# Optimization experiments

Hardware: AMD Instinct MI355X
Metric: run time of the kernel (lower is better)

Reference implementation:

```python
import jax, jax.numpy as jnp
import numpy as np

EPS = 1e-5
K_NUM, EDGE_TYPE = 5, 2  # k_num = A_fixed_partitions(3) + edge_type(2)


def _bn(x, gamma, beta):
    # training-mode BatchNorm2d: batch stats over (N, T, V) per channel
    m = jnp.mean(x, axis=(0, 2, 3), keepdims=True)
    v = jnp.var(x, axis=(0, 2, 3), keepdims=True)
    return (x - m) * jax.lax.rsqrt(v + EPS) * gamma[None, :, None, None] + beta[None, :, None, None]


def setup_inputs() -> dict:
    key = jax.random.key(0)
    ks = jax.random.split(key, 6)
    N, C, T, V = 32, 64, 300, 25
    Cout, Kt = 64, 9
    x = jax.random.normal(ks[0], (N, C, T, V), jnp.float32)
    A = jax.random.uniform(ks[1], (K_NUM - EDGE_TYPE, V, V), jnp.float32) / V  # fixed adjacency (already scaled by edge_importance)
    B = jax.random.uniform(ks[2], (N, EDGE_TYPE, V, V), jnp.float32) / V      # per-sample adaptive adjacency A_act
    lamda_act = jnp.full((1,), 0.5, jnp.float32)
    conv_w = jax.random.normal(ks[3], (Cout * K_NUM, C), jnp.float32) * (1.0 / np.sqrt(C))  # 1x1 conv weight
    conv_b = jnp.zeros((Cout * K_NUM,), jnp.float32)
    bn1_g = jnp.ones((Cout,), jnp.float32)
    bn1_b = jnp.zeros((Cout,), jnp.float32)
    tcn_w = jax.random.normal(ks[4], (Cout, Cout, Kt, 1), jnp.float32) * (1.0 / np.sqrt(Cout * Kt))
    tcn_b = jnp.zeros((Cout,), jnp.float32)
    bn2_g = jnp.ones((Cout,), jnp.float32)
    bn2_b = jnp.zeros((Cout,), jnp.float32)
    return dict(x=x, A=A, B=B, lamda_act=lamda_act, conv_w=conv_w, conv_b=conv_b,
                bn1_g=bn1_g, bn1_b=bn1_b, tcn_w=tcn_w, tcn_b=tcn_b, bn2_g=bn2_g, bn2_b=bn2_b)


def reference(x, A, B, lamda_act, conv_w, conv_b, bn1_g, bn1_b, tcn_w, tcn_b, bn2_g, bn2_b):
    n, c, t, v = x.shape
    res = x  # identity residual (in_ch == out_ch, stride 1)
    # SpatialGcn: 1x1 conv (pure channel GEMM) -> split -> dual einsum graph conv
    y = jnp.einsum('nctv,oc->notv', x, conv_w) + conv_b[None, :, None, None]  # (n, K*Cout, t, v)
    cout = y.shape[1] // K_NUM
    y = y.reshape(n, K_NUM, cout, t, v)
    x1 = jnp.einsum('nkctv,kvw->nctw', y[:, :K_NUM - EDGE_TYPE], A)   # fixed adjacency
    x2 = jnp.einsum('nkctv,nkvw->nctw', y[:, K_NUM - EDGE_TYPE:], B)  # adaptive adjacency
    g = x1 + x2 * lamda_act[0]
    # tcn: BN -> ReLU -> temporal conv (9,1) pad (4,0) -> BN -> Dropout(0)=identity
    h = jax.nn.relu(_bn(g, bn1_g, bn1_b))
    h = jax.lax.conv_general_dilated(h, tcn_w, window_strides=(1, 1),
                                     padding=((4, 4), (0, 0)),
                                     dimension_numbers=('NCHW', 'OIHW', 'NCHW'))
    h = h + tcn_b[None, :, None, None]
    h = _bn(h, bn2_g, bn2_b)
    return jax.nn.relu(h + res)
```

## Files before the change

### kernel.cpp

```cpp
#include <hip/hip_runtime.h>
#include <hip/hip_bf16.h>

#define N_  32
#define C_  64
#define T_  300
#define V_  25
#define TV  (T_*V_)
#define CTV (C_*TV)
#define NELEM (N_*CTV)
#define CNTF 240000.0f

typedef float f32x4 __attribute__((ext_vector_type(4)));
typedef short bf16x8 __attribute__((ext_vector_type(8)));
typedef short s4v __attribute__((ext_vector_type(4)));
typedef short s8v __attribute__((ext_vector_type(8)));

__device__ __forceinline__ unsigned short f2bf(float f) {
    unsigned u = __float_as_uint(f);
    unsigned r = u + 0x7fffu + ((u >> 16) & 1u);
    return (unsigned short)(r >> 16);
}
__device__ __forceinline__ float bf2f(unsigned short u) {
    return __uint_as_float(((unsigned)u) << 16);
}
__device__ __forceinline__ unsigned cvt_pk(float lo, float hi) {
    unsigned r;
    asm("v_cvt_pk_bf16_f32 %0, %1, %2" : "=v"(r) : "v"(lo), "v"(hi));
    return r;
}

__global__ __launch_bounds__(256) void k_prep(
    const float* __restrict__ conv_w, const float* __restrict__ tw,
    unsigned short* __restrict__ w2b, unsigned short* __restrict__ twb)
{
    int tid = blockIdx.x*256 + threadIdx.x;
    for (int e = tid; e < 20480; e += 8192) {
        int ks = e >> 11, c = (e >> 5) & 63, kk = e & 31;
        w2b[e] = f2bf(conv_w[(((ks>>1)*64 + c)*64) + (ks&1)*32 + kk]);
    }
    for (int e = tid; e < 36864; e += 8192) {
        int gi = e >> 11, c = (e >> 5) & 63, kk = e & 31;
        int dt = gi >> 1, ks = gi & 1;
        twb[e] = f2bf(tw[(c*64 + 32*ks + kk)*9 + dt]);
    }
}

__global__ __launch_bounds__(256) void k_gcn(
    const float* __restrict__ x, const float* __restrict__ A,
    const float* __restrict__ B, const float* __restrict__ lamda,
    const unsigned short* __restrict__ w2b, const float* __restrict__ conv_b,
    unsigned short* __restrict__ gout, float* __restrict__ stats3)
{
    __shared__ unsigned short ash[5*32*40];
    __shared__ unsigned short zsh[32*328];
    __shared__ float csum[160];
    __shared__ float sbc[320];

    const int tb = blockIdx.x, n = blockIdx.y;
    const int t0 = tb*10;
    const int tid = threadIdx.x;
    const int lane = tid & 63, wv = tid >> 6;
    const int lg = lane >> 4, lr = lane & 15;
    const int crow = lr + 16*wv;
    const int cbase = 16*wv + 4*lg;

    bf16x8 wfrag[10];
    #pragma unroll
    for (int ks = 0; ks < 10; ++ks)
        wfrag[ks] = *(const bf16x8*)&w2b[(ks*64 + crow)*32 + 8*lg];

    const float lam = lamda[0];
    {
        s8v z8 = {0,0,0,0,0,0,0,0};
        for (int e = tid; e < 800; e += 256) *(s8v*)&ash[e*8] = z8;
    }
    for (int e = tid; e < 320; e += 256) sbc[e] = conv_b[e];
    __syncthreads();
    for (int e = tid; e < 3125; e += 256) {
        int k = e / 625, r = e - k*625;
        int v = r / 25, w = r - v*25;
        float val = (k < 3) ? A[e] : lam * B[((n<<1) + (k-3))*625 + r];
        ash[k*1280 + w*40 + v] = f2bf(val);
    }
    __syncthreads();
    for (int e = tid; e < 160; e += 256) {
        int k = e / 32, w = e % 32;
        float s = 0.f;
        for (int v = 0; v < 25; ++v) s += bf2f(ash[k*1280 + w*40 + v]);
        csum[e] = s;
    }
    __syncthreads();

    float bs0[4], bs1[4];
    #pragma unroll
    for (int r = 0; r < 4; ++r) {
        float s0 = 0.f, s1 = 0.f;
        #pragma unroll
        for (int k = 0; k < 5; ++k) {
            float cb = sbc[k*64 + cbase + r];
            s0 += cb * csum[k*32 + lr];
            s1 += cb * csum[k*32 + lr + 16];
        }
        bs0[r] = s0; bs1[r] = s1;
    }

    float sacc[4] = {0,0,0,0}, qacc[4] = {0,0,0,0};

    const float* xrow = x + n*CTV + crow*TV + t0*V_;
    float xf[8];
    #pragma unroll
    for (int i = 0; i < 8; ++i) { int v = 8*lg + i; xf[i] = (v < 25) ? xrow[v] : 0.f; }

    for (int tl = 0; tl < 10; ++tl) {
        union { bf16x8 v; unsigned u[4]; } xu;
        #pragma unroll
        for (int p = 0; p < 4; ++p) xu.u[p] = cvt_pk(xf[2*p], xf[2*p+1]);
        bf16x8 xfrag = xu.v;
        if (tl < 9) {
            const float* xn = xrow + (tl+1)*V_;
            #pragma unroll
            for (int i = 0; i < 8; ++i) { int v = 8*lg + i; xf[i] = (v < 25) ? xn[v] : 0.f; }
        }
        #pragma unroll
        for (int k = 0; k < 5; ++k)
        #pragma unroll
        for (int nt = 0; nt < 2; ++nt) {
            bf16x8 bfrag = *(const bf16x8*)&ash[k*1280 + (lr + 16*nt)*40 + 8*lg];
            f32x4 z = {0.f,0.f,0.f,0.f};
            z = __builtin_amdgcn_mfma_f32_16x16x32_bf16(xfrag, bfrag, z, 0, 0, 0);
            uint2 zz;
            zz.x = cvt_pk(z[0], z[1]);
            zz.y = cvt_pk(z[2], z[3]);
            *(uint2*)&zsh[(lr + 16*nt)*328 + k*64 + 16*wv + 4*lg] = zz;
        }
        __syncthreads();
        f32x4 acc0 = {0.f,0.f,0.f,0.f}, acc1 = {0.f,0.f,0.f,0.f};
        #pragma unroll
        for (int ks = 0; ks < 10; ++ks) {
            bf16x8 b0 = *(const bf16x8*)&zsh[lr*328 + 32*ks + 8*lg];
            bf16x8 b1 = *(const bf16x8*)&zsh[(lr+16)*328 + 32*ks + 8*lg];
            acc0 = __builtin_amdgcn_mfma_f32_16x16x32_bf16(wfrag[ks], b0, acc0, 0, 0, 0);
            acc1 = __builtin_amdgcn_mfma_f32_16x16x32_bf16(wfrag[ks], b1, acc1, 0, 0, 0);
        }
        float v0a[4], v1a[4];
        #pragma unroll
        for (int r = 0; r < 4; ++r) {
            v0a[r] = acc0[r] + bs0[r];
            v1a[r] = acc1[r] + bs1[r];
            sacc[r] += v0a[r] + (lr < 9 ? v1a[r] : 0.f);
            qacc[r] += v0a[r]*v0a[r] + (lr < 9 ? v1a[r]*v1a[r] : 0.f);
        }
        unsigned short* grow = gout + (size_t)(n*300 + t0 + tl)*1600;
        uint2 g0, g1;
        g0.x = cvt_pk(v0a[0], v0a[1]); g0.y = cvt_pk(v0a[2], v0a[3]);
        g1.x = cvt_pk(v1a[0], v1a[1]); g1.y = cvt_pk(v1a[2], v1a[3]);
        *(uint2*)&grow[lr*64 + cbase] = g0;
        if (lr < 9) *(uint2*)&grow[(lr+16)*64 + cbase] = g1;
        __syncthreads();
    }

    #pragma unroll
    for (int r = 0; r < 4; ++r) {
        float s = sacc[r], q = qacc[r];
        s += __shfl_xor(s, 1); s += __shfl_xor(s, 2);
        s += __shfl_xor(s, 4); s += __shfl_xor(s, 8);
        q += __shfl_xor(q, 1); q += __shfl_xor(q, 2);
        q += __shfl_xor(q, 4); q += __shfl_xor(q, 8);
        if (lr == 0) {
            stats3[(n*30 + tb)*128 + cbase + r] = s;
            stats3[(n*30 + tb)*128 + 64 + cbase + r] = q;
        }
    }
}

__global__ __launch_bounds__(256) void k_fin(
    const float* __restrict__ src, int count, float* __restrict__ sbo,
    const float* __restrict__ gma, const float* __restrict__ bta)
{
    const int c = blockIdx.x, tid = threadIdx.x;
    float s = 0.f, q = 0.f;
    for (int b = tid; b < count; b += 256) {
        s += src[b*128 + c];
        q += src[b*128 + 64 + c];
    }
    #pragma unroll
    for (int m = 1; m < 64; m <<= 1) { s += __shfl_xor(s, m); q += __shfl_xor(q, m); }
    __shared__ float rs[4], rq[4];
    if ((tid & 63) == 0) { rs[tid>>6] = s; rq[tid>>6] = q; }
    __syncthreads();
    if (tid == 0) {
        s = rs[0]+rs[1]+rs[2]+rs[3]; q = rq[0]+rq[1]+rq[2]+rq[3];
        float mean = s / CNTF, var = q / CNTF - mean*mean;
        float sc = gma[c] * rsqrtf(var + 1e-5f);
        sbo[c] = sc;
        sbo[64 + c] = bta[c] - mean*sc;
    }
}

__global__ __launch_bounds__(512, 4) void k_tcn(
    const unsigned short* __restrict__ gin, const float* __restrict__ sb,
    const unsigned short* __restrict__ twb, const float* __restrict__ tb,
    unsigned short* __restrict__ hout, float* __restrict__ stats4)
{
    __shared__ unsigned short pT[400*40];
    __shared__ float sbs[128];

    const int n = blockIdx.y, tt = blockIdx.x, t0 = tt*8;
    const int tid = threadIdx.x;
    const int lane = tid & 63, wv = tid >> 6;
    const int lg = lane >> 4, lr = lane & 15;
    const int ct = wv & 3, ch = wv >> 2;
    const int cfrag = ct*16 + lr;
    const int cbase = ct*16 + 4*lg;

    for (int e = tid; e < 128; e += 512) sbs[e] = sb[e];

    f32x4 acc[7];
    #pragma unroll
    for (int i = 0; i < 7; ++i) acc[i] = (f32x4){0.f,0.f,0.f,0.f};

    for (int ks = 0; ks < 2; ++ks) {
        bf16x8 af[9];
        #pragma unroll
        for (int dt = 0; dt < 9; ++dt)
            af[dt] = *(const bf16x8*)&twb[((dt*2 + ks)*64 + cfrag)*32 + 8*lg];

        __syncthreads();
        for (int e8 = tid; e8 < 1600; e8 += 512) {
            int tl = e8 / 100, r = e8 % 100, w = r >> 2, c8 = r & 3;
            int tg = t0 - 4 + tl;
            int i8 = 32*ks + c8*8;
            uint4 packed = {0,0,0,0};
            if (tg >= 0 && tg < 300) {
                s8v raw = *(const s8v*)&gin[(size_t)((n*300 + tg)*25 + w)*64 + i8];
                float f[8];
                #pragma unroll
                for (int j = 0; j < 8; ++j)
                    f[j] = fmaxf(fmaf(bf2f((unsigned short)raw[j]), sbs[i8+j], sbs[64+i8+j]), 0.f);
                packed.x = cvt_pk(f[0], f[1]);
                packed.y = cvt_pk(f[2], f[3]);
                packed.z = cvt_pk(f[4], f[5]);
                packed.w = cvt_pk(f[6], f[7]);
            }
            *(uint4*)&pT[(tl*25 + w)*40 + c8*8] = packed;
        }
        __syncthreads();

        #pragma unroll
        for (int i = 0; i < 7; ++i) {
            int col = lr + 16*(ch*7 + i); if (col > 199) col = 199;
            #pragma unroll
            for (int dt = 0; dt < 9; ++dt) {
                bf16x8 b = *(const bf16x8*)&pT[(col + 25*dt)*40 + 8*lg];
                acc[i] = __builtin_amdgcn_mfma_f32_16x16x32_bf16(af[dt], b, acc[i], 0, 0, 0);
            }
        }
    }

    const int lim = min(200, (300 - t0)*25);
    float tbc[4];
    #pragma unroll
    for (int r = 0; r < 4; ++r) tbc[r] = tb[cbase + r];

    float sacc[4] = {0,0,0,0}, qacc[4] = {0,0,0,0};
    #pragma unroll
    for (int i = 0; i < 7; ++i) {
        int col = lr + 16*(ch*7 + i);
        if (col < lim) {
            #pragma unroll
            for (int r = 0; r < 4; ++r) {
                float v = acc[i][r] + tbc[r];
                sacc[r] += v; qacc[r] += v*v;
            }
        }
    }
    #pragma unroll
    for (int r = 0; r < 4; ++r) {
        float s = sacc[r], q = qacc[r];
        s += __shfl_xor(s, 1); s += __shfl_xor(s, 2);
        s += __shfl_xor(s, 4); s += __shfl_xor(s, 8);
        q += __shfl_xor(q, 1); q += __shfl_xor(q, 2);
        q += __shfl_xor(q, 4); q += __shfl_xor(q, 8);
        if (lr == 0) {
            float* dst = stats4 + (size_t)((n*38 + tt)*2 + ch)*128;
            dst[cbase + r] = s;
            dst[64 + cbase + r] = q;
        }
    }

    __syncthreads();
    unsigned short* hbuf = pT;
    #pragma unroll
    for (int i = 0; i < 7; ++i) {
        int col = lr + 16*(ch*7 + i);
        if (col < 200) {
            #pragma unroll
            for (int r = 0; r < 4; ++r)
                hbuf[(cbase + r)*200 + col] = f2bf(acc[i][r] + tbc[r]);
        }
    }
    __syncthreads();
    for (int e = tid; e < 3200; e += 512) {
        int row = e / 50, c4 = (e % 50)*4;
        if (c4 < lim) {
            s4v o = *(const s4v*)&hbuf[row*200 + c4];
            *(s4v*)&hout[((size_t)(n*64 + row)*300 + t0)*25 + c4] = o;
        }
    }
}

__global__ __launch_bounds__(256) void k_out(
    const unsigned short* __restrict__ h, const float* __restrict__ x,
    const float* __restrict__ sb, float* __restrict__ out)
{
    int i4 = blockIdx.x * 256 + threadIdx.x;
    if (i4 >= NELEM/4) return;
    int c = ((i4*4) / TV) & 63;
    float s2 = sb[128 + c], b2 = sb[192 + c];
    s4v hv = *(const s4v*)&h[i4*4];
    float4 xv = ((const float4*)x)[i4];
    float4 o;
    o.x = fmaxf(fmaf(bf2f((unsigned short)hv[0]), s2, b2) + xv.x, 0.f);
    o.y = fmaxf(fmaf(bf2f((unsigned short)hv[1]), s2, b2) + xv.y, 0.f);
    o.z = fmaxf(fmaf(bf2f((unsigned short)hv[2]), s2, b2) + xv.z, 0.f);
    o.w = fmaxf(fmaf(bf2f((unsigned short)hv[3]), s2, b2) + xv.w, 0.f);
    ((float4*)out)[i4] = o;
}

extern "C" void kernel_launch(void* const* d_in, const int* in_sizes, int n_in,
                              void* d_out, int out_size, void* d_ws, size_t ws_size,
                              hipStream_t stream)
{
    const float* x      = (const float*)d_in[0];
    const float* A      = (const float*)d_in[1];
    const float* B      = (const float*)d_in[2];
    const float* lamda  = (const float*)d_in[3];
    const float* conv_w = (const float*)d_in[4];
    const float* conv_b = (const float*)d_in[5];
    const float* bn1_g  = (const float*)d_in[6];
    const float* bn1_b  = (const float*)d_in[7];
    const float* tcn_w  = (const float*)d_in[8];
    const float* tcn_b  = (const float*)d_in[9];
    const float* bn2_g  = (const float*)d_in[10];
    const float* bn2_b  = (const float*)d_in[11];

    unsigned short* g = (unsigned short*)d_ws;
    unsigned short* h = g + NELEM;
    float* stats3 = (float*)(h + NELEM);
    float* stats4 = stats3 + 960*128;
    float* sb     = stats4 + 2432*128;
    unsigned short* w2b = (unsigned short*)(sb + 256);
    unsigned short* twb = w2b + 20480;

    k_prep<<<32, 256, 0, stream>>>(conv_w, tcn_w, w2b, twb);
    k_gcn<<<dim3(30, N_), 256, 0, stream>>>(x, A, B, lamda, w2b, conv_b, g, stats3);
    k_fin<<<64, 256, 0, stream>>>(stats3, 960, sb, bn1_g, bn1_b);
    k_tcn<<<dim3(38, N_), 512, 0, stream>>>(g, sb, twb, tcn_b, h, stats4);
    k_fin<<<64, 256, 0, stream>>>(stats4, 2432, sb + 128, bn2_g, bn2_b);
    k_out<<<NELEM/4/256, 256, 0, stream>>>(h, x, sb, (float*)d_out);
}
```

Measured before the change: 134.7 us.

## Split BN1+ReLU into padded pre-pass and retile temporal conv over flat T*V

Moves the BN1 scale/shift and ReLU out of the temporal-conv kernel into a separate elementwise kernel. That kernel writes a zero-padded bf16 buffer, which removes the boundary checks. The tcn kernel now tiles 128 flattened (t,v) columns per 256-thread block, loads all 64 input channels into XOR-swizzled LDS once with a single sync, and runs both K halves without reloading. The aim is to cut redundant halo conversion and LDS bank conflicts and raise MFMA density. The cost is an extra global round trip for the padded activation buffer and one more launch.

```diff
diff --git a/kernel.cpp b/kernel.cpp
--- a/kernel.cpp
+++ b/kernel.cpp
@@ -9,6 +9,7 @@
 #define CTV (C_*TV)
 #define NELEM (N_*CTV)
 #define CNTF 240000.0f
+#define PROWS 7788
 
 typedef float f32x4 __attribute__((ext_vector_type(4)));
 typedef short bf16x8 __attribute__((ext_vector_type(8)));
@@ -197,79 +198,87 @@
     }
 }
 
-__global__ __launch_bounds__(512, 4) void k_tcn(
-    const unsigned short* __restrict__ gin, const float* __restrict__ sb,
-    const unsigned short* __restrict__ twb, const float* __restrict__ tb,
-    unsigned short* __restrict__ hout, float* __restrict__ stats4)
-{
-    __shared__ unsigned short pT[400*40];
+__global__ __launch_bounds__(256) void k_bn1(
+    const unsigned short* __restrict__ g, const float* __restrict__ sb,
+    unsigned short* __restrict__ p)
+{
     __shared__ float sbs[128];
-
-    const int n = blockIdx.y, tt = blockIdx.x, t0 = tt*8;
+    if (threadIdx.x < 128) sbs[threadIdx.x] = sb[threadIdx.x];
+    __syncthreads();
+    int idx = blockIdx.x*256 + threadIdx.x;
+    int n = idx / (PROWS*8);
+    int rem = idx - n*(PROWS*8);
+    int row = (rem >> 3) - 128;
+    int q8 = (rem & 7) * 8;
+    uint4 out4 = {0,0,0,0};
+    if (row >= 0 && row < 7500) {
+        s8v raw = *(const s8v*)&g[((size_t)n*7500 + row)*64 + q8];
+        float f[8];
+        #pragma unroll
+        for (int j = 0; j < 8; ++j)
+            f[j] = fmaxf(fmaf(bf2f((unsigned short)raw[j]), sbs[q8+j], sbs[64+q8+j]), 0.f);
+        out4.x = cvt_pk(f[0], f[1]); out4.y = cvt_pk(f[2], f[3]);
+        out4.z = cvt_pk(f[4], f[5]); out4.w = cvt_pk(f[6], f[7]);
+    }
+    *(uint4*)&p[(size_t)idx*8] = out4;
+}
+
+__global__ __launch_bounds__(256) void k_tcn(
+    const unsigned short* __restrict__ p, const unsigned short* __restrict__ twb,
+    const float* __restrict__ tb, unsigned short* __restrict__ hout,
+    float* __restrict__ stats4)
+{
+    __shared__ unsigned short lds[328*64];
+
+    const int bj = blockIdx.x, n = blockIdx.y;
+    const int j0 = bj*128;
     const int tid = threadIdx.x;
-    const int lane = tid & 63, wv = tid >> 6;
+    const int lane = tid & 63, ct = tid >> 6;
     const int lg = lane >> 4, lr = lane & 15;
-    const int ct = wv & 3, ch = wv >> 2;
-    const int cfrag = ct*16 + lr;
+    const int cA = ct*16 + lr;
     const int cbase = ct*16 + 4*lg;
 
-    for (int e = tid; e < 128; e += 512) sbs[e] = sb[e];
-
-    f32x4 acc[7];
-    #pragma unroll
-    for (int i = 0; i < 7; ++i) acc[i] = (f32x4){0.f,0.f,0.f,0.f};
-
+    const unsigned short* psrc = p + ((size_t)n*PROWS + 28 + j0)*64;
+    for (int e = tid; e < 2624; e += 256) {
+        int row = e >> 3, q = e & 7;
+        s8v v = *(const s8v*)&psrc[(size_t)row*64 + q*8];
+        *(s8v*)&lds[row*64 + ((q ^ (row & 7)))*8] = v;
+    }
+
+    f32x4 acc[8];
+    #pragma unroll
+    for (int i = 0; i < 8; ++i) acc[i] = (f32x4){0.f,0.f,0.f,0.f};
+    float tbc[4];
+    #pragma unroll
+    for (int r = 0; r < 4; ++r) tbc[r] = tb[cbase + r];
+
+    __syncthreads();
+
+    #pragma unroll
     for (int ks = 0; ks < 2; ++ks) {
         bf16x8 af[9];
         #pragma unroll
         for (int dt = 0; dt < 9; ++dt)
-            af[dt] = *(const bf16x8*)&twb[((dt*2 + ks)*64 + cfrag)*32 + 8*lg];
-
-        __syncthreads();
-        for (int e8 = tid; e8 < 1600; e8 += 512) {
-            int tl = e8 / 100, r = e8 % 100, w = r >> 2, c8 = r & 3;
-            int tg = t0 - 4 + tl;
-            int i8 = 32*ks + c8*8;
-            uint4 packed = {0,0,0,0};
-            if (tg >= 0 && tg < 300) {
-                s8v raw = *(const s8v*)&gin[(size_t)((n*300 + tg)*25 + w)*64 + i8];
-                float f[8];
-                #pragma unroll
-                for (int j = 0; j < 8; ++j)
-                    f[j] = fmaxf(fmaf(bf2f((unsigned short)raw[j]), sbs[i8+j], sbs[64+i8+j]), 0.f);
-                packed.x = cvt_pk(f[0], f[1]);
-                packed.y = cvt_pk(f[2], f[3]);
-                packed.z = cvt_pk(f[4], f[5]);
-                packed.w = cvt_pk(f[6], f[7]);
-            }
-            *(uint4*)&pT[(tl*25 + w)*40 + c8*8] = packed;
-        }
-        __syncthreads();
-
-        #pragma unroll
-        for (int i = 0; i < 7; ++i) {
-            int col = lr + 16*(ch*7 + i); if (col > 199) col = 199;
+            af[dt] = *(const bf16x8*)&twb[((2*dt + ks)*64 + cA)*32 + 8*lg];
+        #pragma unroll
+        for (int jt = 0; jt < 8; ++jt) {
             #pragma unroll
             for (int dt = 0; dt < 9; ++dt) {
-                bf16x8 b = *(const bf16x8*)&pT[(col + 25*dt)*40 + 8*lg];
-                acc[i] = __builtin_amdgcn_mfma_f32_16x16x32_bf16(af[dt], b, acc[i], 0, 0, 0);
+                int row = 16*jt + lr + 25*dt;
+                bf16x8 b = *(const bf16x8*)&lds[row*64 + ((4*ks + lg) ^ (row & 7))*8];
+                acc[jt] = __builtin_amdgcn_mfma_f32_16x16x32_bf16(af[dt], b, acc[jt], 0, 0, 0);
             }
         }
     }
 
-    const int lim = min(200, (300 - t0)*25);
-    float tbc[4];
-    #pragma unroll
-    for (int r = 0; r < 4; ++r) tbc[r] = tb[cbase + r];
-
     float sacc[4] = {0,0,0,0}, qacc[4] = {0,0,0,0};
     #pragma unroll
-    for (int i = 0; i < 7; ++i) {
-        int col = lr + 16*(ch*7 + i);
-        if (col < lim) {
+    for (int jt = 0; jt < 8; ++jt) {
+        int j = j0 + 16*jt + lr;
+        if (j < 7500) {
             #pragma unroll
             for (int r = 0; r < 4; ++r) {
-                float v = acc[i][r] + tbc[r];
+                float v = acc[jt][r] + tbc[r];
                 sacc[r] += v; qacc[r] += v*v;
             }
         }
@@ -282,30 +291,24 @@
         q += __shfl_xor(q, 1); q += __shfl_xor(q, 2);
         q += __shfl_xor(q, 4); q += __shfl_xor(q, 8);
         if (lr == 0) {
-            float* dst = stats4 + (size_t)((n*38 + tt)*2 + ch)*128;
+            float* dst = stats4 + (size_t)(n*59 + bj)*128;
             dst[cbase + r] = s;
             dst[64 + cbase + r] = q;
         }
     }
 
     __syncthreads();
-    unsigned short* hbuf = pT;
-    #pragma unroll
-    for (int i = 0; i < 7; ++i) {
-        int col = lr + 16*(ch*7 + i);
-        if (col < 200) {
-            #pragma unroll
-            for (int r = 0; r < 4; ++r)
-                hbuf[(cbase + r)*200 + col] = f2bf(acc[i][r] + tbc[r]);
-        }
-    }
-    __syncthreads();
-    for (int e = tid; e < 3200; e += 512) {
-        int row = e / 50, c4 = (e % 50)*4;
-        if (c4 < lim) {
-            s4v o = *(const s4v*)&hbuf[row*200 + c4];
-            *(s4v*)&hout[((size_t)(n*64 + row)*300 + t0)*25 + c4] = o;
-        }
+    #pragma unroll
+    for (int jt = 0; jt < 8; ++jt)
+        #pragma unroll
+        for (int r = 0; r < 4; ++r)
+            lds[(cbase + r)*136 + 16*jt + lr] = f2bf(acc[jt][r] + tbc[r]);
+    __syncthreads();
+    for (int e = tid; e < 2048; e += 256) {
+        int row = e >> 5, c4 = (e & 31) << 2;
+        int j = j0 + c4;
+        if (j < 7500)
+            *(s4v*)&hout[(size_t)(n*64 + row)*7500 + j] = *(const s4v*)&lds[row*136 + c4];
     }
 }
 
@@ -345,17 +348,19 @@
     const float* bn2_b  = (const float*)d_in[11];
 
     unsigned short* g = (unsigned short*)d_ws;
-    unsigned short* h = g + NELEM;
+    unsigned short* p = g + NELEM;
+    unsigned short* h = p + (size_t)N_*PROWS*64;
     float* stats3 = (float*)(h + NELEM);
     float* stats4 = stats3 + 960*128;
-    float* sb     = stats4 + 2432*128;
+    float* sb     = stats4 + 1888*128;
     unsigned short* w2b = (unsigned short*)(sb + 256);
     unsigned short* twb = w2b + 20480;
 
     k_prep<<<32, 256, 0, stream>>>(conv_w, tcn_w, w2b, twb);
     k_gcn<<<dim3(30, N_), 256, 0, stream>>>(x, A, B, lamda, w2b, conv_b, g, stats3);
     k_fin<<<64, 256, 0, stream>>>(stats3, 960, sb, bn1_g, bn1_b);
-    k_tcn<<<dim3(38, N_), 512, 0, stream>>>(g, sb, twb, tcn_b, h, stats4);
-    k_fin<<<64, 256, 0, stream>>>(stats4, 2432, sb + 128, bn2_g, bn2_b);
+    k_bn1<<<PROWS, 256, 0, stream>>>(g, sb, p);
+    k_tcn<<<dim3(59, N_), 256, 0, stream>>>(p, twb, tcn_b, h, stats4);
+    k_fin<<<64, 256, 0, stream>>>(stats4, 1888, sb + 128, bn2_g, bn2_b);
     k_out<<<NELEM/4/256, 256, 0, stream>>>(h, x, sb, (float*)d_out);
 }
```

Measured after the change: 134.6 us. About the same (-0.1%).
